# Performance work log

Measured on AMD Instinct MI355X. Metric: run time of the kernel, lower is better.

## Reference

```python
import jax, jax.numpy as jnp
import numpy as np

B, C, H, W = 8, 256, 64, 64
NH, D = 4, 64
BLKQ = BLKK = 64
TOPK_RATIO = 0.1
EPS = 1e-6


def setup_inputs() -> dict:
    key = jax.random.key(0)
    k1, k2, k3, k4, k5 = jax.random.split(key, 5)
    x = jax.random.normal(k1, (B, C, H, W), dtype=jnp.float32)
    qkv_w = jax.random.normal(k2, (3 * C, C), dtype=jnp.float32) / np.sqrt(C)
    out_w = jax.random.normal(k3, (C, C), dtype=jnp.float32) / np.sqrt(C)
    # NOTE: the torch module zero-inits proj_l and out_proj (output would be
    # identically zero); we use small random weights for a useful baseline.
    proj_lw = jax.random.normal(k4, (D, D), dtype=jnp.float32) * 0.02
    proj_lb = jax.random.normal(k5, (D,), dtype=jnp.float32) * 0.02
    return {"x": x, "qkv_w": qkv_w, "out_w": out_w, "proj_lw": proj_lw, "proj_lb": proj_lb}


def _sla_forward(x, qkv_w, out_w, proj_lw, proj_lb):
    Bn, Cn, Hn, Wn = x.shape
    L = Hn * Wn
    nQ, nK = L // BLKQ, L // BLKK
    T = max(1, int(TOPK_RATIO * nK))  # real_topk = 6
    xf = x.reshape(Bn, Cn, L)
    qkv = jnp.einsum('oc,bcl->bol', qkv_w, xf)  # 1x1 conv, no bias
    q, k, v = jnp.split(qkv, 3, axis=1)
    # (B, C, L) -> (B, H, L, D)
    def to_bhld(t):
        return t.reshape(Bn, NH, D, L).transpose(0, 1, 3, 2)
    q, k, v = to_bhld(q), to_bhld(k), to_bhld(v)

    # ---- block-level top-k map (get_block_map) ----
    qr = q.reshape(Bn, NH, nQ, BLKQ, D)
    kr = k.reshape(Bn, NH, nK, BLKK, D)
    vr = v.reshape(Bn, NH, nK, BLKK, D)
    qb = qr.mean(axis=3)                       # (B,H,nQ,D)
    kb = kr.mean(axis=3)                       # (B,H,nK,D)
    blk_scores = jnp.einsum('bhnd,bhmd->bhnm', qb, kb)
    _, lut = jax.lax.top_k(blk_scores, T)      # (B,H,nQ,T)

    # ---- sparse path: softmax attention over gathered top-k key blocks ----
    idx = lut[..., None, None]                 # (B,H,nQ,T,1,1)
    kg = jnp.take_along_axis(kr[:, :, None], idx, axis=3)  # (B,H,nQ,T,BLKK,D)
    vg = jnp.take_along_axis(vr[:, :, None], idx, axis=3)
    kg = kg.reshape(Bn, NH, nQ, T * BLKK, D)
    vg = vg.reshape(Bn, NH, nQ, T * BLKK, D)
    scale = D ** -0.5
    s = jnp.einsum('bhnqd,bhnkd->bhnqk', qr, kg) * scale
    p = jax.nn.softmax(s, axis=-1)
    o_s = jnp.einsum('bhnqk,bhnkd->bhnqd', p, vg)          # (B,H,nQ,BLKQ,D)

    # ---- linear path over complement (non-selected) key blocks ----
    c_q = jax.nn.softmax(q, axis=-1)           # feature_map='softmax'
    c_k = jax.nn.softmax(k, axis=-1)
    c_kr = c_k.reshape(Bn, NH, nK, BLKK, D)
    kvb = jnp.einsum('bhmkd,bhmke->bhmde', c_kr, vr)       # (B,H,nK,D,D)
    ksum = c_kr.sum(axis=3)                                # (B,H,nK,D)
    sel = jax.nn.one_hot(lut, nK, dtype=q.dtype).sum(axis=3)  # (B,H,nQ,nK)
    comp = 1.0 - sel
    kv_q = jnp.einsum('bhnm,bhmde->bhnde', comp, kvb)
    ks_q = jnp.einsum('bhnm,bhmd->bhnd', comp, ksum)
    c_qr = c_q.reshape(Bn, NH, nQ, BLKQ, D)
    num = jnp.einsum('bhnqd,bhnde->bhnqe', c_qr, kv_q)
    den = jnp.einsum('bhnqd,bhnd->bhnq', c_qr, ks_q)
    o_l = num / (den[..., None] + EPS)

    o_l = jnp.einsum('bhnqd,ed->bhnqe', o_l, proj_lw) + proj_lb
    o = (o_s + o_l).reshape(Bn, NH, L, D)
    o = o.transpose(0, 1, 3, 2).reshape(Bn, Cn, L)
    o = jnp.einsum('oc,bcl->bol', out_w, o)    # out_proj 1x1 conv
    return o.reshape(Bn, Cn, Hn, Wn)


def reference(x, qkv_w, out_w, proj_lw, proj_lb):
    return _sla_forward(x, qkv_w, out_w, proj_lw, proj_lb)
```

## Files before the change

### kernel.cpp

```cpp
#include <hip/hip_runtime.h>
#include <hip/hip_bf16.h>
#include <cmath>

#define NB 8
#define NC 256
#define NHH 4
#define DD 64
#define LL 4096
#define NQ 64
#define NKB 64
#define BLK 64
#define TT 6
#define PAD 72

typedef _Float16 f16;
typedef _Float16 half8 __attribute__((ext_vector_type(8)));
typedef float f32x4 __attribute__((ext_vector_type(4)));
typedef unsigned int uint4v __attribute__((ext_vector_type(4)));
typedef unsigned long long ull;

#define INV2048 4.8828125e-4f

union H4 { f16 h[4]; ull u; };
union H2 { f16 h[2]; unsigned int u; };

#define MFMA16(A, B, C) __builtin_amdgcn_mfma_f32_16x16x32_f16(A, B, C, 0, 0, 0)

__global__ void qbkb_kernel(const float* __restrict__ w, const float* __restrict__ xb,
                            float* __restrict__ qb, float* __restrict__ kb) {
  int id = blockIdx.x;
  int h = id % NHH; id /= NHH;
  int n = id % NQ;  int b = id / NQ;
  int t = threadIdx.x;
  int d = t & 63;
  int part = t >> 6;
  const float* wrow = w + (size_t)(part * NC + h * DD + d) * NC;
  const float* xcol = xb + (size_t)b * NC * NQ + n;
  float acc = 0.f;
#pragma unroll 4
  for (int c = 0; c < NC; ++c) acc += wrow[c] * xcol[(size_t)c * NQ];
  float* dst = (part == 0) ? qb : kb;
  dst[(((size_t)b * NHH + h) * NQ + n) * DD + d] = acc;
}

__global__ void topk_kernel(const float* __restrict__ qb, const float* __restrict__ kb,
                            int* __restrict__ lut) {
  __shared__ float kbs[NKB][DD + 1];
  int id = blockIdx.x;
  int n = id % NQ;
  int bh = id / NQ;
  int m = threadIdx.x;
  const float* kbp = kb + (size_t)bh * NKB * DD;
  for (int i = threadIdx.x; i < NKB * DD; i += 64) kbs[i >> 6][i & 63] = kbp[i];
  __syncthreads();
  const float* qrow = qb + ((size_t)bh * NQ + n) * DD;
  float s = 0.f;
#pragma unroll 8
  for (int d2 = 0; d2 < DD; ++d2) s += qrow[d2] * kbs[m][d2];
  for (int t = 0; t < TT; ++t) {
    float v = s; int i = m;
#pragma unroll
    for (int off = 1; off < 64; off <<= 1) {
      float ov = __shfl_xor(v, off);
      int oi = __shfl_xor(i, off);
      if (ov > v || (ov == v && oi < i)) { v = ov; i = oi; }
    }
    if (m == 0) lut[(size_t)id * TT + t] = i;
    if (m == i) s = -INFINITY;
  }
}

__global__ void wsplit_kernel(const float* __restrict__ wq, const float* __restrict__ wo,
                              const float* __restrict__ plw,
                              f16* __restrict__ wqh,
                              f16* __restrict__ woh, f16* __restrict__ wol,
                              f16* __restrict__ plwh, f16* __restrict__ plwl) {
  int blk = blockIdx.x;
  if (blk < 192) {
    int i = (blk * 256 + threadIdx.x) * 4;
    float4 v = *(const float4*)(wq + i);
    H4 hh;
    hh.h[0] = (f16)v.x; hh.h[1] = (f16)v.y; hh.h[2] = (f16)v.z; hh.h[3] = (f16)v.w;
    *(ull*)(wqh + i) = hh.u;
    return;
  }
  const float* src; f16* dh; f16* dl; int n;
  if (blk < 256) { src = wo;  dh = woh;  dl = wol;  n = NC * NC; blk -= 192; }
  else           { src = plw; dh = plwh; dl = plwl; n = DD * DD; blk -= 256; }
  int i = (blk * 256 + threadIdx.x) * 4;
  if (i >= n) return;
  float4 v = *(const float4*)(src + i);
  H4 hh, ll;
  hh.h[0] = (f16)v.x; ll.h[0] = (f16)((v.x - (float)hh.h[0]) * 2048.f);
  hh.h[1] = (f16)v.y; ll.h[1] = (f16)((v.y - (float)hh.h[1]) * 2048.f);
  hh.h[2] = (f16)v.z; ll.h[2] = (f16)((v.z - (float)hh.h[2]) * 2048.f);
  hh.h[3] = (f16)v.w; ll.h[3] = (f16)((v.w - (float)hh.h[3]) * 2048.f);
  *(ull*)(dh + i) = hh.u;
  *(ull*)(dl + i) = ll.u;
}

__global__ __launch_bounds__(256) void xsplit_kernel(const float* __restrict__ x,
                                                     f16* __restrict__ xh,
                                                     float* __restrict__ xb) {
  __shared__ float T[64][65];
  int l0 = blockIdx.x * 64, c0 = blockIdx.y * 64, b = blockIdx.z;
  int tid = threadIdx.x;
  for (int it = 0; it < 16; ++it) {
    int idx = it * 256 + tid; int c = idx >> 6, l = idx & 63;
    T[c][l] = x[((size_t)b * NC + c0 + c) * LL + l0 + l];
  }
  __syncthreads();
  {
    int c = tid >> 2, qq = tid & 3;
    float s = 0.f;
#pragma unroll
    for (int l = 0; l < 16; ++l) s += T[c][qq * 16 + l];
    s += __shfl_xor(s, 1);
    s += __shfl_xor(s, 2);
    if (qq == 0) xb[((size_t)b * NC + c0 + c) * NQ + blockIdx.x] = s * (1.f / 64.f);
  }
  for (int it = 0; it < 4; ++it) {
    int idx = it * 256 + tid; int l = idx >> 4, cq = idx & 15;
    H4 hh;
    hh.h[0] = (f16)T[cq * 4 + 0][l];
    hh.h[1] = (f16)T[cq * 4 + 1][l];
    hh.h[2] = (f16)T[cq * 4 + 2][l];
    hh.h[3] = (f16)T[cq * 4 + 3][l];
    *(ull*)(xh + ((size_t)b * LL + l0 + l) * NC + c0 + cq * 4) = hh.u;
  }
}

__global__ __launch_bounds__(256) void qkv_fused(
    const f16* __restrict__ xh,
    const f16* __restrict__ wh,
    f16* __restrict__ qh,
    f16* __restrict__ kh, f16* __restrict__ vT,
    f16* __restrict__ kvbT, float* __restrict__ ksum) {
  __shared__ f16 XH[BLK][PAD];
  __shared__ f16 VS[BLK][PAD];
  int L = blockIdx.x;
  int b = L & 7;
  int t = L >> 3;
  int l0 = (t >> 2) * 64;
  int h = t & 3;
  int m = l0 >> 6;
  int tid = threadIdx.x;
  int w = tid >> 6, lane = tid & 63, c16 = lane & 15, g = lane >> 4;
  f32x4 accq[4], acck[4], accv[4];
#pragma unroll
  for (int j = 0; j < 4; ++j) {
    accq[j] = (f32x4){0.f,0.f,0.f,0.f};
    acck[j] = (f32x4){0.f,0.f,0.f,0.f};
    accv[j] = (f32x4){0.f,0.f,0.f,0.f};
  }
  size_t wqbase = (size_t)(h * DD + w * 16 + c16) * NC;
  size_t wkbase = (size_t)(NC + h * DD + w * 16 + c16) * NC;
  size_t wvbase = (size_t)(2 * NC + h * DD + w * 16 + c16) * NC;
  for (int c0 = 0; c0 < NC; c0 += 64) {
    __syncthreads();
#pragma unroll
    for (int it = 0; it < 2; ++it) {
      int idx = it * 256 + tid; int pos = idx >> 3, dp8 = idx & 7;
      size_t gsrc = ((size_t)b * LL + l0 + pos) * NC + c0 + dp8 * 8;
      *(uint4v*)&XH[pos][dp8 * 8] = *(const uint4v*)(xh + gsrc);
    }
    __syncthreads();
#pragma unroll
    for (int ks = 0; ks < 2; ++ks) {
      half8 awq = *(const half8*)(wh + wqbase + c0 + ks * 32 + g * 8);
      half8 awk = *(const half8*)(wh + wkbase + c0 + ks * 32 + g * 8);
      half8 awv = *(const half8*)(wh + wvbase + c0 + ks * 32 + g * 8);
#pragma unroll
      for (int j = 0; j < 4; ++j) {
        half8 bxh = *(const half8*)&XH[j * 16 + c16][ks * 32 + g * 8];
        accq[j] = MFMA16(awq, bxh, accq[j]);
        acck[j] = MFMA16(awk, bxh, acck[j]);
        accv[j] = MFMA16(awv, bxh, accv[j]);
      }
    }
  }
  int bh = b * NHH + h;
#pragma unroll
  for (int j = 0; j < 4; ++j) {
    H4 hq, hk;
#pragma unroll
    for (int r = 0; r < 4; ++r) { hq.h[r] = (f16)accq[j][r]; hk.h[r] = (f16)acck[j][r]; }
    size_t off = ((size_t)bh * LL + l0 + j * 16 + c16) * DD + w * 16 + g * 4;
    *(ull*)(qh + off) = hq.u;
    *(ull*)(kh + off) = hk.u;
  }
  __syncthreads();
#pragma unroll
  for (int j = 0; j < 4; ++j)
#pragma unroll
    for (int r = 0; r < 4; ++r) {
      XH[j * 16 + c16][w * 16 + g * 4 + r] = (f16)acck[j][r];
      VS[j * 16 + c16][w * 16 + g * 4 + r] = (f16)accv[j][r];
    }
  __syncthreads();
#pragma unroll
  for (int it = 0; it < 4; ++it) {
    int idx = it * 256 + tid; int d = idx >> 4, p4 = (idx & 15) * 4;
    H4 hh;
    hh.h[0] = VS[p4 + 0][d]; hh.h[1] = VS[p4 + 1][d];
    hh.h[2] = VS[p4 + 2][d]; hh.h[3] = VS[p4 + 3][d];
    *(ull*)(vT + ((size_t)bh * DD + d) * LL + l0 + p4) = hh.u;
  }
  {
    int r = tid >> 2, p = tid & 3;
    float v[16];
    float mx = -INFINITY;
#pragma unroll
    for (int c = 0; c < 16; ++c) { v[c] = (float)XH[r][p * 16 + c]; mx = fmaxf(mx, v[c]); }
    mx = fmaxf(mx, __shfl_xor(mx, 1));
    mx = fmaxf(mx, __shfl_xor(mx, 2));
    float sum = 0.f;
#pragma unroll
    for (int c = 0; c < 16; ++c) { v[c] = __expf(v[c] - mx); sum += v[c]; }
    sum += __shfl_xor(sum, 1);
    sum += __shfl_xor(sum, 2);
    float inv = 1.0f / sum;
#pragma unroll
    for (int c = 0; c < 16; ++c) XH[r][p * 16 + c] = (f16)(v[c] * inv);
  }
  __syncthreads();
  if (tid < DD) {
    float s = 0.f;
#pragma unroll 8
    for (int j = 0; j < BLK; ++j) s += (float)XH[j][tid];
    ksum[((size_t)bh * NKB + m) * DD + tid] = s;
  }
  int tx = tid & 15, ty = tid >> 4;
  float acc[4][4] = {};
#pragma unroll 4
  for (int j = 0; j < BLK; ++j) {
    H4 va = *(H4*)&VS[j][ty * 4];
    H4 ca = *(H4*)&XH[j][tx * 4];
    float a[4], bb[4];
#pragma unroll
    for (int i = 0; i < 4; ++i) { a[i] = (float)va.h[i]; bb[i] = (float)ca.h[i]; }
#pragma unroll
    for (int i = 0; i < 4; ++i)
#pragma unroll
      for (int jj = 0; jj < 4; ++jj) acc[i][jj] += a[i] * bb[jj];
  }
  f16* dst = kvbT + ((size_t)bh * NKB + m) * DD * DD;
#pragma unroll
  for (int i = 0; i < 4; ++i) {
    H4 hh;
#pragma unroll
    for (int jj = 0; jj < 4; ++jj) hh.h[jj] = (f16)acc[i][jj];
    *(ull*)(dst + (size_t)(ty * 4 + i) * DD + tx * 4) = hh.u;
  }
}

__global__ void totals_kernel(const f16* __restrict__ kvbT, const float* __restrict__ ksum,
                              float* __restrict__ kvtot, float* __restrict__ kstot) {
  int bi = blockIdx.x;
  int bh = bi >> 4, s = bi & 15;
  int tid = threadIdx.x;
  int i = s * 256 + tid;
  float acc = 0.f;
  const f16* src = kvbT + (size_t)bh * NKB * DD * DD + i;
  for (int m2 = 0; m2 < NKB; ++m2) acc += (float)src[(size_t)m2 * DD * DD];
  kvtot[(size_t)bh * DD * DD + i] = acc;
  if (s == 0 && tid < DD) {
    float ss = 0.f;
    for (int m2 = 0; m2 < NKB; ++m2) ss += ksum[((size_t)bh * NKB + m2) * DD + tid];
    kstot[(size_t)bh * DD + tid] = ss;
  }
}

__global__ __launch_bounds__(256) void attn_mfma(
    const f16* __restrict__ qh_g,
    const f16* __restrict__ kh_g, const f16* __restrict__ vT_g,
    const f16* __restrict__ kvbT, const float* __restrict__ ksum,
    const float* __restrict__ kvtot, const float* __restrict__ kstot,
    const int* __restrict__ lut,
    const f16* __restrict__ plwh, const f16* __restrict__ plwl,
    const float* __restrict__ plb,
    f16* __restrict__ och) {
  __shared__ f16 KH[BLK][PAD], VH[BLK][PAD], PH[BLK][PAD];
  __shared__ float ksq[DD], dinv[BLK];
  int L = blockIdx.x;
  int rest = L >> 3;
  int bh = (L & 7) * 4 + (rest >> 6);
  int n = rest & 63;
  int id = bh * NQ + n;
  int b = bh >> 2, h = bh & 3;
  int tid = threadIdx.x;
  int w = tid >> 6, lane = tid & 63, c16 = lane & 15, g = lane >> 4;
  int lu[TT];
#pragma unroll
  for (int t = 0; t < TT; ++t) lu[t] = lut[(size_t)id * TT + t];
  size_t qbase = ((size_t)bh * LL + (size_t)n * BLK + w * 16 + c16) * DD;
  half8 bqh[2];
#pragma unroll
  for (int ks = 0; ks < 2; ++ks) bqh[ks] = *(const half8*)(qh_g + qbase + ks * 32 + g * 8);
  f32x4 acco[4];
#pragma unroll
  for (int j = 0; j < 4; ++j) acco[j] = (f32x4){0.f,0.f,0.f,0.f};
  float l_run = 0.f;
  uint4v kreg[2], vreg[2];
  {
    int mb = lu[0];
#pragma unroll
    for (int it = 0; it < 2; ++it) {
      int idx = it * 256 + tid; int pos = idx >> 3, dp8 = idx & 7;
      kreg[it] = *(const uint4v*)(kh_g + ((size_t)bh * LL + (size_t)mb * BLK + pos) * DD + dp8 * 8);
      vreg[it] = *(const uint4v*)(vT_g + ((size_t)bh * DD + pos) * LL + (size_t)mb * BLK + dp8 * 8);
    }
  }
  for (int t = 0; t < TT; ++t) {
    __syncthreads();
#pragma unroll
    for (int it = 0; it < 2; ++it) {
      int idx = it * 256 + tid; int pos = idx >> 3, dp8 = idx & 7;
      *(uint4v*)&KH[pos][dp8 * 8] = kreg[it];
      *(uint4v*)&VH[pos][dp8 * 8] = vreg[it];
    }
    __syncthreads();
    if (t + 1 < TT) {
      int mb = lu[t + 1];
#pragma unroll
      for (int it = 0; it < 2; ++it) {
        int idx = it * 256 + tid; int pos = idx >> 3, dp8 = idx & 7;
        kreg[it] = *(const uint4v*)(kh_g + ((size_t)bh * LL + (size_t)mb * BLK + pos) * DD + dp8 * 8);
        vreg[it] = *(const uint4v*)(vT_g + ((size_t)bh * DD + pos) * LL + (size_t)mb * BLK + dp8 * 8);
      }
    }
    float rs = 0.f;
#pragma unroll
    for (int i = 0; i < 4; ++i) {
      f32x4 acc = {0.f, 0.f, 0.f, 0.f};
#pragma unroll
      for (int ks = 0; ks < 2; ++ks) {
        half8 ah = *(const half8*)&KH[i * 16 + c16][ks * 32 + g * 8];
        acc = MFMA16(ah, bqh[ks], acc);
      }
      H4 pp;
#pragma unroll
      for (int r = 0; r < 4; ++r) {
        float p = __expf(acc[r] * 0.125f - 4.f);
        rs += p;
        pp.h[r] = (f16)p;
      }
      *(ull*)&PH[w * 16 + c16][i * 16 + g * 4] = pp.u;
    }
    rs += __shfl_xor(rs, 16);
    rs += __shfl_xor(rs, 32);
    l_run += rs;
#pragma unroll
    for (int ks = 0; ks < 2; ++ks) {
      half8 pb = *(const half8*)&PH[w * 16 + c16][ks * 32 + g * 8];
#pragma unroll
      for (int j = 0; j < 4; ++j) {
        half8 vhf = *(const half8*)&VH[j * 16 + c16][ks * 32 + g * 8];
        acco[j] = MFMA16(vhf, pb, acco[j]);
      }
    }
  }
  __syncthreads();
  float linv = 1.f / l_run;
#pragma unroll
  for (int j = 0; j < 4; ++j)
#pragma unroll
    for (int r = 0; r < 4; ++r) acco[j][r] *= linv;
  if (tid < DD) {
    float s = kstot[(size_t)bh * DD + tid];
#pragma unroll
    for (int t2 = 0; t2 < TT; ++t2) s -= ksum[((size_t)bh * NKB + lu[t2]) * DD + tid];
    ksq[tid] = s;
  }
  int cr = tid >> 2, cp = tid & 3;
  float cq[16];
  {
    size_t qrow = ((size_t)bh * LL + (size_t)n * BLK + cr) * DD + cp * 16;
    half8 qa = *(const half8*)(qh_g + qrow), qa2 = *(const half8*)(qh_g + qrow + 8);
#pragma unroll
    for (int c = 0; c < 8; ++c) {
      cq[c] = (float)qa[c];
      cq[8 + c] = (float)qa2[c];
    }
    float mx2 = -INFINITY;
#pragma unroll
    for (int c = 0; c < 16; ++c) mx2 = fmaxf(mx2, cq[c]);
    mx2 = fmaxf(mx2, __shfl_xor(mx2, 1));
    mx2 = fmaxf(mx2, __shfl_xor(mx2, 2));
    float sum = 0.f;
#pragma unroll
    for (int c = 0; c < 16; ++c) { cq[c] = __expf(cq[c] - mx2); sum += cq[c]; }
    sum += __shfl_xor(sum, 1);
    sum += __shfl_xor(sum, 2);
    float inv = 1.f / sum;
#pragma unroll
    for (int c = 0; c < 16; ++c) cq[c] *= inv;
  }
#pragma unroll
  for (int c = 0; c < 8; ++c) {
    H2 hh;
    hh.h[0] = (f16)cq[2 * c];
    hh.h[1] = (f16)cq[2 * c + 1];
    *(unsigned int*)&VH[cr][cp * 16 + 2 * c] = hh.u;
  }
  {
    const float* kvtp = kvtot + (size_t)bh * DD * DD;
    const f16* kvbp = kvbT + (size_t)bh * NKB * DD * DD;
    for (int it = 0; it < 16; ++it) {
      int idx = it * 256 + tid;
      int dd2 = idx & 63, e = idx >> 6;
      float s = kvtp[e * DD + dd2];
#pragma unroll
      for (int t2 = 0; t2 < TT; ++t2)
        s -= (float)kvbp[(size_t)lu[t2] * DD * DD + e * DD + dd2];
      KH[e][dd2] = (f16)s;
    }
  }
  __syncthreads();
  {
    float dpart = 0.f;
#pragma unroll
    for (int c = 0; c < 16; ++c) dpart += cq[c] * ksq[cp * 16 + c];
    dpart += __shfl_xor(dpart, 1);
    dpart += __shfl_xor(dpart, 2);
    if (cp == 0) dinv[cr] = 1.f / (dpart + 1e-6f);
  }
  f32x4 accn[4];
  {
    half8 cqh[2];
#pragma unroll
    for (int ks = 0; ks < 2; ++ks)
      cqh[ks] = *(const half8*)&VH[w * 16 + c16][ks * 32 + g * 8];
#pragma unroll
    for (int j = 0; j < 4; ++j) {
      f32x4 acc = {0.f, 0.f, 0.f, 0.f};
#pragma unroll
      for (int ks = 0; ks < 2; ++ks) {
        half8 ah = *(const half8*)&KH[j * 16 + c16][ks * 32 + g * 8];
        acc = MFMA16(ah, cqh[ks], acc);
      }
      accn[j] = acc;
    }
  }
  __syncthreads();
  float di = dinv[w * 16 + c16];
#pragma unroll
  for (int j = 0; j < 4; ++j) {
    float o0 = accn[j][0] * di;
    float o1 = accn[j][1] * di;
    float o2 = accn[j][2] * di;
    float o3 = accn[j][3] * di;
    H4 hh, ll;
    hh.h[0] = (f16)o0; ll.h[0] = (f16)((o0 - (float)hh.h[0]) * 2048.f);
    hh.h[1] = (f16)o1; ll.h[1] = (f16)((o1 - (float)hh.h[1]) * 2048.f);
    hh.h[2] = (f16)o2; ll.h[2] = (f16)((o2 - (float)hh.h[2]) * 2048.f);
    hh.h[3] = (f16)o3; ll.h[3] = (f16)((o3 - (float)hh.h[3]) * 2048.f);
    *(ull*)&PH[w * 16 + c16][j * 16 + g * 4] = hh.u;
    *(ull*)&KH[w * 16 + c16][j * 16 + g * 4] = ll.u;
  }
  f32x4 accf2[4];
#pragma unroll
  for (int j = 0; j < 4; ++j) accf2[j] = (f32x4){0.f,0.f,0.f,0.f};
#pragma unroll
  for (int ks = 0; ks < 2; ++ks) {
    half8 bolh = *(const half8*)&PH[w * 16 + c16][ks * 32 + g * 8];
    half8 boll = *(const half8*)&KH[w * 16 + c16][ks * 32 + g * 8];
#pragma unroll
    for (int j = 0; j < 4; ++j) {
      size_t pwoff = (size_t)(j * 16 + c16) * DD + ks * 32 + g * 8;
      half8 awh = *(const half8*)(plwh + pwoff);
      half8 awl = *(const half8*)(plwl + pwoff);
      acco[j]  = MFMA16(awh, bolh, acco[j]);
      accf2[j] = MFMA16(awh, boll, accf2[j]);
      accf2[j] = MFMA16(awl, bolh, accf2[j]);
    }
  }
  size_t obase = ((size_t)b * LL + (size_t)n * BLK + w * 16 + c16) * NC + h * DD;
#pragma unroll
  for (int j = 0; j < 4; ++j) {
    H4 hh;
#pragma unroll
    for (int r = 0; r < 4; ++r) {
      int e2 = j * 16 + g * 4 + r;
      hh.h[r] = (f16)(acco[j][r] + accf2[j][r] * INV2048 + plb[e2]);
    }
    *(ull*)(och + obase + j * 16 + g * 4) = hh.u;
  }
}

__global__ __launch_bounds__(256) void out_mfma(
    const f16* __restrict__ och,
    const f16* __restrict__ wh, const f16* __restrict__ wl,
    float* __restrict__ out) {
  __shared__ f16 OH[BLK][PAD];
  int l0 = blockIdx.x * 64;
  int o0 = blockIdx.y * 64;
  int b = blockIdx.z;
  int tid = threadIdx.x;
  int w = tid >> 6, lane = tid & 63, c16 = lane & 15, g = lane >> 4;
  f32x4 acc[4], acc2[4];
#pragma unroll
  for (int j = 0; j < 4; ++j) { acc[j] = (f32x4){0.f,0.f,0.f,0.f}; acc2[j] = (f32x4){0.f,0.f,0.f,0.f}; }
  size_t wbase = (size_t)(o0 + w * 16 + c16) * NC;
  for (int c0 = 0; c0 < NC; c0 += 64) {
    __syncthreads();
#pragma unroll
    for (int it = 0; it < 2; ++it) {
      int idx = it * 256 + tid; int pos = idx >> 3, dp8 = idx & 7;
      size_t gsrc = ((size_t)b * LL + l0 + pos) * NC + c0 + dp8 * 8;
      *(uint4v*)&OH[pos][dp8 * 8] = *(const uint4v*)(och + gsrc);
    }
    __syncthreads();
#pragma unroll
    for (int ks = 0; ks < 2; ++ks) {
      half8 awh = *(const half8*)(wh + wbase + c0 + ks * 32 + g * 8);
      half8 awl = *(const half8*)(wl + wbase + c0 + ks * 32 + g * 8);
#pragma unroll
      for (int j = 0; j < 4; ++j) {
        half8 bh = *(const half8*)&OH[j * 16 + c16][ks * 32 + g * 8];
        acc[j]  = MFMA16(awh, bh, acc[j]);
        acc2[j] = MFMA16(awl, bh, acc2[j]);
      }
    }
  }
#pragma unroll
  for (int j = 0; j < 4; ++j)
#pragma unroll
    for (int r = 0; r < 4; ++r)
      out[((size_t)b * NC + o0 + w * 16 + g * 4 + r) * LL + l0 + j * 16 + c16] =
          acc[j][r] + acc2[j][r] * INV2048;
}

extern "C" void kernel_launch(void* const* d_in, const int* in_sizes, int n_in,
                              void* d_out, int out_size, void* d_ws, size_t ws_size,
                              hipStream_t stream) {
  (void)in_sizes; (void)n_in; (void)out_size; (void)ws_size;
  const float* x = (const float*)d_in[0];
  const float* qkv_w = (const float*)d_in[1];
  const float* out_w = (const float*)d_in[2];
  const float* plw = (const float*)d_in[3];
  const float* plb = (const float*)d_in[4];
  float* out = (float*)d_out;
  const size_t E = (size_t)NB * NHH * LL * DD;
  f16* fb = (f16*)d_ws;
  f16* qh = fb;
  f16* kh = qh + E;
  f16* vT = kh + E;
  f16* xTh = vT + E;
  f16* och = xTh;
  f16* kvbT = xTh + E;
  float* fbase = (float*)(kvbT + E);
  float* ksum = fbase;
  float* kvtot = ksum + (size_t)NB * NHH * NKB * DD;
  float* kstot = kvtot + (size_t)NB * NHH * DD * DD;
  float* xb = kstot + (size_t)NB * NHH * DD;
  float* qb = xb + (size_t)NB * NC * NQ;
  float* kb = qb + (size_t)NB * NHH * NQ * DD;
  int* lut = (int*)(kb + (size_t)NB * NHH * NQ * DD);
  f16* wqh = (f16*)(lut + (size_t)NB * NHH * NQ * TT);
  f16* woh = wqh + (size_t)3 * NC * NC;
  f16* wol = woh + (size_t)NC * NC;
  f16* plwh = wol + (size_t)NC * NC;
  f16* plwl = plwh + (size_t)DD * DD;

  xsplit_kernel<<<dim3(LL / 64, NC / 64, NB), 256, 0, stream>>>(x, xTh, xb);
  qbkb_kernel<<<NB * NQ * NHH, 128, 0, stream>>>(qkv_w, xb, qb, kb);
  topk_kernel<<<NB * NHH * NQ, 64, 0, stream>>>(qb, kb, lut);
  wsplit_kernel<<<260, 256, 0, stream>>>(qkv_w, out_w, plw, wqh, woh, wol, plwh, plwl);
  qkv_fused<<<LL / 64 * NHH * NB, 256, 0, stream>>>(xTh, wqh, qh, kh, vT, kvbT, ksum);
  totals_kernel<<<NB * NHH * 16, 256, 0, stream>>>(kvbT, ksum, kvtot, kstot);
  attn_mfma<<<NB * NHH * NQ, 256, 0, stream>>>(qh, kh, vT, kvbT, ksum,
                                               kvtot, kstot, lut, plwh, plwl, plb,
                                               och);
  out_mfma<<<dim3(LL / 64, NC / 64, NB), 256, 0, stream>>>(och, woh, wol, out);
}
```

Before: 177.4 us.

## Fold complement KV subtraction into MFMA via negated query features

In attn_mfma, the complement KV matrix is no longer built in shared memory as the total minus the selected blocks. The code now runs MFMAs of cq against the f16 total KV, then adds MFMAs of -cq against each of the six selected block KVs, reading those directly from global memory. The per-block scalar gather-subtract loop is gone, and the totals are stored in f16 rather than f32. This costs seven times as many MFMAs for this product and gives up the f32 accumulation of the subtraction, which can hurt accuracy through cancellation.

```diff
diff --git a/kernel.cpp b/kernel.cpp
--- a/kernel.cpp
+++ b/kernel.cpp
@@ -255,7 +255,7 @@
 }
 
 __global__ void totals_kernel(const f16* __restrict__ kvbT, const float* __restrict__ ksum,
-                              float* __restrict__ kvtot, float* __restrict__ kstot) {
+                              f16* __restrict__ kvtotH, float* __restrict__ kstot) {
   int bi = blockIdx.x;
   int bh = bi >> 4, s = bi & 15;
   int tid = threadIdx.x;
@@ -263,7 +263,7 @@
   float acc = 0.f;
   const f16* src = kvbT + (size_t)bh * NKB * DD * DD + i;
   for (int m2 = 0; m2 < NKB; ++m2) acc += (float)src[(size_t)m2 * DD * DD];
-  kvtot[(size_t)bh * DD * DD + i] = acc;
+  kvtotH[(size_t)bh * DD * DD + i] = (f16)acc;
   if (s == 0 && tid < DD) {
     float ss = 0.f;
     for (int m2 = 0; m2 < NKB; ++m2) ss += ksum[((size_t)bh * NKB + m2) * DD + tid];
@@ -275,7 +275,7 @@
     const f16* __restrict__ qh_g,
     const f16* __restrict__ kh_g, const f16* __restrict__ vT_g,
     const f16* __restrict__ kvbT, const float* __restrict__ ksum,
-    const float* __restrict__ kvtot, const float* __restrict__ kstot,
+    const f16* __restrict__ kvtotH, const float* __restrict__ kstot,
     const int* __restrict__ lut,
     const f16* __restrict__ plwh, const f16* __restrict__ plwl,
     const float* __restrict__ plb,
@@ -398,23 +398,13 @@
   }
 #pragma unroll
   for (int c = 0; c < 8; ++c) {
-    H2 hh;
+    H2 hh, nn;
     hh.h[0] = (f16)cq[2 * c];
     hh.h[1] = (f16)cq[2 * c + 1];
+    nn.h[0] = (f16)(-cq[2 * c]);
+    nn.h[1] = (f16)(-cq[2 * c + 1]);
     *(unsigned int*)&VH[cr][cp * 16 + 2 * c] = hh.u;
-  }
-  {
-    const float* kvtp = kvtot + (size_t)bh * DD * DD;
-    const f16* kvbp = kvbT + (size_t)bh * NKB * DD * DD;
-    for (int it = 0; it < 16; ++it) {
-      int idx = it * 256 + tid;
-      int dd2 = idx & 63, e = idx >> 6;
-      float s = kvtp[e * DD + dd2];
-#pragma unroll
-      for (int t2 = 0; t2 < TT; ++t2)
-        s -= (float)kvbp[(size_t)lu[t2] * DD * DD + e * DD + dd2];
-      KH[e][dd2] = (f16)s;
-    }
+    *(unsigned int*)&PH[cr][cp * 16 + 2 * c] = nn.u;
   }
   __syncthreads();
   {
@@ -427,19 +417,33 @@
   }
   f32x4 accn[4];
   {
-    half8 cqh[2];
+    half8 cqh[2], cqn[2];
+#pragma unroll
+    for (int ks = 0; ks < 2; ++ks) {
+      cqh[ks] = *(const half8*)&VH[w * 16 + c16][ks * 32 + g * 8];
+      cqn[ks] = *(const half8*)&PH[w * 16 + c16][ks * 32 + g * 8];
+    }
+#pragma unroll
+    for (int j = 0; j < 4; ++j) accn[j] = (f32x4){0.f,0.f,0.f,0.f};
+    const f16* tp = kvtotH + (size_t)bh * DD * DD;
 #pragma unroll
     for (int ks = 0; ks < 2; ++ks)
-      cqh[ks] = *(const half8*)&VH[w * 16 + c16][ks * 32 + g * 8];
-#pragma unroll
-    for (int j = 0; j < 4; ++j) {
-      f32x4 acc = {0.f, 0.f, 0.f, 0.f};
-#pragma unroll
-      for (int ks = 0; ks < 2; ++ks) {
-        half8 ah = *(const half8*)&KH[j * 16 + c16][ks * 32 + g * 8];
-        acc = MFMA16(ah, cqh[ks], acc);
-      }
-      accn[j] = acc;
+#pragma unroll
+      for (int j = 0; j < 4; ++j) {
+        half8 at = *(const half8*)(tp + (size_t)(j * 16 + c16) * DD + ks * 32 + g * 8);
+        accn[j] = MFMA16(at, cqh[ks], accn[j]);
+      }
+    const f16* kvbp = kvbT + (size_t)bh * NKB * DD * DD;
+#pragma unroll
+    for (int t2 = 0; t2 < TT; ++t2) {
+      const f16* kp = kvbp + (size_t)lu[t2] * DD * DD;
+#pragma unroll
+      for (int ks = 0; ks < 2; ++ks)
+#pragma unroll
+        for (int j = 0; j < 4; ++j) {
+          half8 ab = *(const half8*)(kp + (size_t)(j * 16 + c16) * DD + ks * 32 + g * 8);
+          accn[j] = MFMA16(ab, cqn[ks], accn[j]);
+        }
     }
   }
   __syncthreads();
@@ -549,10 +553,10 @@
   f16* xTh = vT + E;
   f16* och = xTh;
   f16* kvbT = xTh + E;
-  float* fbase = (float*)(kvbT + E);
+  f16* kvtotH = kvbT + E;
+  float* fbase = (float*)(kvtotH + (size_t)NB * NHH * DD * DD);
   float* ksum = fbase;
-  float* kvtot = ksum + (size_t)NB * NHH * NKB * DD;
-  float* kstot = kvtot + (size_t)NB * NHH * DD * DD;
+  float* kstot = ksum + (size_t)NB * NHH * NKB * DD;
   float* xb = kstot + (size_t)NB * NHH * DD;
   float* qb = xb + (size_t)NB * NC * NQ;
   float* kb = qb + (size_t)NB * NHH * NQ * DD;
@@ -568,9 +572,9 @@
   topk_kernel<<<NB * NHH * NQ, 64, 0, stream>>>(qb, kb, lut);
   wsplit_kernel<<<260, 256, 0, stream>>>(qkv_w, out_w, plw, wqh, woh, wol, plwh, plwl);
   qkv_fused<<<LL / 64 * NHH * NB, 256, 0, stream>>>(xTh, wqh, qh, kh, vT, kvbT, ksum);
-  totals_kernel<<<NB * NHH * 16, 256, 0, stream>>>(kvbT, ksum, kvtot, kstot);
+  totals_kernel<<<NB * NHH * 16, 256, 0, stream>>>(kvbT, ksum, kvtotH, kstot);
   attn_mfma<<<NB * NHH * NQ, 256, 0, stream>>>(qh, kh, vT, kvbT, ksum,
-                                               kvtot, kstot, lut, plwh, plwl, plb,
+                                               kvtotH, kstot, lut, plwh, plwl, plb,
                                                och);
   out_mfma<<<dim3(LL / 64, NC / 64, NB), 256, 0, stream>>>(och, woh, wol, out);
 }
```

Result: slower. 214.9 us (+21.1%).
